# Optimization experiments

Measured on AMD Instinct MI355X. Metric: run time of the kernel, lower is better.

## Reference

```python
import jax, jax.numpy as jnp
import numpy as np

WAY = 5
SHOT = 5
SCALE = 10.0
EPS = 1e-8


def setup_inputs() -> dict:
    key = jax.random.key(0)
    k1, k2 = jax.random.split(key, 2)
    x = jax.random.normal(k1, (100, 512, 16, 16), dtype=jnp.float32)
    W = jax.random.normal(k2, (512, 512), dtype=jnp.float32) * 0.02  # 1x1 conv weight (outC, inC)
    b = jnp.zeros((512,), dtype=jnp.float32)
    return {"x": x, "W": W, "b": b}


def reference(x, W, b):
    B, C, H, Wd = x.shape
    # extract(): 1x1 conv -> softmax over flattened (C*H*W) per sample -> remask
    mask = jnp.einsum('bchw,oc->bohw', x, W) + b[None, :, None, None]
    mask = jax.nn.softmax(mask.reshape(B, -1), axis=1).reshape(B, C, H, Wd)
    x = x * mask
    # predict(): (way, shot+query, C, H, W)
    xv = x.reshape(WAY, -1, C, H, Wd)
    s = xv[:, :SHOT].mean(axis=(1, 3, 4))                    # (m=way, d=C) support prototypes
    q = xv[:, SHOT:].reshape(-1, C, H * Wd)                  # (n, d=C, f=H*W) queries
    # cosine_similarity over d, without materializing (n,m,d,f)
    qn = jnp.maximum(jnp.sqrt(jnp.sum(q * q, axis=1)), EPS)  # (n, f)
    sn = jnp.maximum(jnp.sqrt(jnp.sum(s * s, axis=1)), EPS)  # (m,)
    scores = jnp.einsum('ndf,md->nmf', q, s) / (qn[:, None, :] * sn[None, :, None])
    # softmax over classes (m), then mean over spatial positions f
    return jax.nn.softmax(SCALE * scores, axis=1).mean(axis=2)  # (n, way)
```

## Files before the change

### kernel.cpp

```cpp
#include <hip/hip_runtime.h>
#include <hip/hip_bf16.h>
#include <math.h>

typedef _Float16 half8 __attribute__((ext_vector_type(8)));
typedef float f32x4 __attribute__((ext_vector_type(4)));

#define BATCH 100
#define CH    512
#define HWP   256
#define SAMP  (CH * HWP)

__device__ __forceinline__ void async16(const void* g, void* l) {
  __builtin_amdgcn_global_load_lds(
      (const __attribute__((address_space(1))) unsigned int*)g,
      (__attribute__((address_space(3))) unsigned int*)l, 16, 0, 0);
}

__global__ __launch_bounds__(256) void k_txpose(const float* __restrict__ x,
                                               _Float16* __restrict__ xh) {
  __shared__ float tb[64][69];
  int bid  = blockIdx.x;
  int b    = bid >> 5;
  int tile = bid & 31;
  int c0 = (tile >> 2) << 6;
  int p0 = (tile & 3) << 6;
  int t = threadIdx.x;
  const float* xb = x + (size_t)b * SAMP;
#pragma unroll
  for (int it = 0; it < 4; it++) {
    int ch = it * 256 + t;
    int c  = ch >> 4;
    int pc = (ch & 15) << 2;
    float4 v = *(const float4*)(xb + (size_t)(c0 + c) * HWP + p0 + pc);
    tb[c][pc] = v.x; tb[c][pc + 1] = v.y; tb[c][pc + 2] = v.z; tb[c][pc + 3] = v.w;
  }
  __syncthreads();
  _Float16* xhb = xh + (size_t)b * SAMP;
#pragma unroll
  for (int it = 0; it < 2; it++) {
    int ch = it * 256 + t;
    int p  = ch >> 3;
    int ck = (ch & 7) << 3;
    half8 h;
#pragma unroll
    for (int j = 0; j < 8; j++) h[j] = (_Float16)tb[ck + j][p];
    *(half8*)(xhb + (size_t)(p0 + p) * CH + c0 + ck) = h;
  }
}

__global__ __launch_bounds__(256) void k_convw(const float* __restrict__ W,
                                              _Float16* __restrict__ Wh) {
  int base = blockIdx.x * 1024 + threadIdx.x;
#pragma unroll
  for (int j = 0; j < 4; j++) Wh[base + j * 256] = (_Float16)W[base + j * 256];
}

__global__ __launch_bounds__(256) void k_gemm(const _Float16* __restrict__ Wh,
                                             const _Float16* __restrict__ xh,
                                             const float* __restrict__ bias,
                                             float* __restrict__ eout,
                                             float* __restrict__ denom) {
  __shared__ __align__(16) _Float16 As[128 * 32];
  __shared__ __align__(16) _Float16 Bs[128 * 32];
  int bid   = blockIdx.x;
  int batch = bid >> 3;
  int sub   = bid & 7;
  int ot = sub & 3, pt = sub >> 2;
  int o0 = ot * 128, p0 = pt * 128;
  const _Float16* Bg = xh + (size_t)batch * SAMP;

  int t  = threadIdx.x;
  int wv = t >> 6, ln = t & 63;
  int qd = ln >> 4, r = ln & 15;
  int wm0 = (wv >> 1) * 64, wn0 = (wv & 1) * 64;

  f32x4 acc[4][4] = {};

  for (int kk = 0; kk < 512; kk += 32) {
#pragma unroll
    for (int it = 0; it < 2; it++) {
      int ch  = it * 256 + t;
      int row = ch >> 2;
      int qc  = ch & 3;
      char* la = (char*)As + (size_t)(it * 256 + wv * 64) * 16;
      char* lb = (char*)Bs + (size_t)(it * 256 + wv * 64) * 16;
      async16((const char*)(Wh + (size_t)(o0 + row) * 512 + kk + qc * 8), la);
      async16((const char*)(Bg + (size_t)(p0 + row) * 512 + kk + qc * 8), lb);
    }
    __syncthreads();
    half8 af[4], bf[4];
#pragma unroll
    for (int i = 0; i < 4; i++)
      af[i] = *(const half8*)(As + (wm0 + i * 16 + r) * 32 + qd * 8);
#pragma unroll
    for (int j = 0; j < 4; j++)
      bf[j] = *(const half8*)(Bs + (wn0 + j * 16 + r) * 32 + qd * 8);
#pragma unroll
    for (int i = 0; i < 4; i++)
#pragma unroll
      for (int j = 0; j < 4; j++)
        acc[i][j] = __builtin_amdgcn_mfma_f32_16x16x32_f16(af[i], bf[j], acc[i][j], 0, 0, 0);
    __syncthreads();
  }

  float* outb = eout + (size_t)batch * SAMP;
  float lsum = 0.f;
#pragma unroll
  for (int i = 0; i < 4; i++) {
#pragma unroll
    for (int rg = 0; rg < 4; rg++) {
      int o = o0 + wm0 + i * 16 + qd * 4 + rg;
      float bv = bias[o];
#pragma unroll
      for (int j = 0; j < 4; j++) {
        int p = p0 + wn0 + j * 16 + r;
        float e = __expf(acc[i][j][rg] + bv);
        outb[(size_t)o * HWP + p] = e;
        lsum += e;
      }
    }
  }
#pragma unroll
  for (int off = 32; off; off >>= 1) lsum += __shfl_down(lsum, off, 64);
  __shared__ float rs[4];
  if (ln == 0) rs[wv] = lsum;
  __syncthreads();
  if (t == 0) atomicAdd(&denom[batch], rs[0] + rs[1] + rs[2] + rs[3]);
}

__global__ __launch_bounds__(256) void k_proto(const float* __restrict__ x,
                                              const float* __restrict__ e,
                                              const float* __restrict__ denom,
                                              float* __restrict__ sproto) {
  int m = blockIdx.x / 512, c = blockIdx.x % 512;
  int t = threadIdx.x;
  float acc = 0.f;
  for (int j = 0; j < 5; j++) {
    int b = m * 20 + j;
    float invd = 1.0f / denom[b];
    size_t idx = (size_t)b * SAMP + (size_t)c * HWP + t;
    acc += x[idx] * e[idx] * invd;
  }
#pragma unroll
  for (int off = 32; off; off >>= 1) acc += __shfl_down(acc, off, 64);
  __shared__ float rs[4];
  if ((t & 63) == 0) rs[t >> 6] = acc;
  __syncthreads();
  if (t == 0) sproto[m * 512 + c] = (rs[0] + rs[1] + rs[2] + rs[3]) * (1.0f / 1280.0f);
}

__global__ __launch_bounds__(256) void k_sn(const float* __restrict__ sproto,
                                           float* __restrict__ pref) {
  int m = blockIdx.x, t = threadIdx.x;
  float v1 = sproto[m * 512 + t], v2 = sproto[m * 512 + 256 + t];
  float acc = v1 * v1 + v2 * v2;
#pragma unroll
  for (int off = 32; off; off >>= 1) acc += __shfl_down(acc, off, 64);
  __shared__ float rs[4];
  if ((t & 63) == 0) rs[t >> 6] = acc;
  __syncthreads();
  if (t == 0) {
    float sn = fmaxf(sqrtf(rs[0] + rs[1] + rs[2] + rs[3]), 1e-8f);
    pref[m] = 10.0f / sn;
  }
}

__global__ __launch_bounds__(256) void k_part(const float* __restrict__ x,
                                             const float* __restrict__ e,
                                             const float* __restrict__ sproto,
                                             float* __restrict__ part) {
  __shared__ float s_l[5 * 32];
  int n = blockIdx.x >> 4, gc = blockIdx.x & 15;
  int b = (n / 15) * 20 + 5 + (n % 15);
  int t = threadIdx.x;
  int c0 = gc * 32;
  if (t < 160) s_l[t] = sproto[(t / 32) * 512 + c0 + (t % 32)];
  __syncthreads();
  const float* xb = x + (size_t)b * SAMP + (size_t)c0 * HWP;
  const float* eb = e + (size_t)b * SAMP + (size_t)c0 * HWP;
  float dot[5] = {0, 0, 0, 0, 0}, qq = 0.f;
#pragma unroll 8
  for (int c = 0; c < 32; c++) {
    float u = xb[c * HWP + t] * eb[c * HWP + t];
    qq += u * u;
#pragma unroll
    for (int m = 0; m < 5; m++) dot[m] += u * s_l[m * 32 + c];
  }
  float* pp = part + (((size_t)n * 16 + gc) * 256 + t) * 6;
  pp[0] = dot[0]; pp[1] = dot[1]; pp[2] = dot[2];
  pp[3] = dot[3]; pp[4] = dot[4]; pp[5] = qq;
}

__global__ __launch_bounds__(256) void k_comb(const float* __restrict__ part,
                                             const float* __restrict__ pref,
                                             float* __restrict__ out) {
  int n = blockIdx.x, t = threadIdx.x;
  float dot[5] = {0, 0, 0, 0, 0}, qq = 0.f;
#pragma unroll
  for (int gc = 0; gc < 16; gc++) {
    const float* pp = part + (((size_t)n * 16 + gc) * 256 + t) * 6;
    dot[0] += pp[0]; dot[1] += pp[1]; dot[2] += pp[2];
    dot[3] += pp[3]; dot[4] += pp[4]; qq += pp[5];
  }
  float iqn = 1.0f / fmaxf(sqrtf(qq), 1e-20f);
  float sc[5], mx = -1e30f;
#pragma unroll
  for (int m = 0; m < 5; m++) { sc[m] = dot[m] * pref[m] * iqn; mx = fmaxf(mx, sc[m]); }
  float p[5], ssum = 0.f;
#pragma unroll
  for (int m = 0; m < 5; m++) { p[m] = __expf(sc[m] - mx); ssum += p[m]; }
  float rr = 1.0f / ssum;
#pragma unroll
  for (int m = 0; m < 5; m++) {
    float v = p[m] * rr;
#pragma unroll
    for (int off = 32; off; off >>= 1) v += __shfl_down(v, off, 64);
    p[m] = v;
  }
  __shared__ float rs[4][5];
  if ((t & 63) == 0) {
#pragma unroll
    for (int m = 0; m < 5; m++) rs[t >> 6][m] = p[m];
  }
  __syncthreads();
  if (t < 5) out[n * 5 + t] =
      (rs[0][t] + rs[1][t] + rs[2][t] + rs[3][t]) * (1.0f / 256.0f);
}

extern "C" void kernel_launch(void* const* d_in, const int* in_sizes, int n_in,
                              void* d_out, int out_size, void* d_ws, size_t ws_size,
                              hipStream_t stream) {
  const float* x    = (const float*)d_in[0];
  const float* W    = (const float*)d_in[1];
  const float* bias = (const float*)d_in[2];
  float* out = (float*)d_out;

  char* ws = (char*)d_ws;
  _Float16* xh     = (_Float16*)(ws + 0);
  float*    part   = (float*)   (ws + 0);
  _Float16* Wh     = (_Float16*)(ws + 26214400);
  float*    e      = (float*)   (ws + 26738688);
  float*    denom  = (float*)   (ws + 79167488);
  float*    sproto = (float*)   (ws + 79168000);
  float*    pref   = (float*)   (ws + 79178240);

  hipMemsetAsync(denom, 0, 512, stream);
  k_txpose <<<3200, 256, 0, stream>>>(x, xh);
  k_convw  <<<256,  256, 0, stream>>>(W, Wh);
  k_gemm   <<<800,  256, 0, stream>>>(Wh, xh, bias, e, denom);
  k_proto  <<<2560, 256, 0, stream>>>(x, e, denom, sproto);
  k_sn     <<<5,    256, 0, stream>>>(sproto, pref);
  k_part   <<<1200, 256, 0, stream>>>(x, e, sproto, part);
  k_comb   <<<75,   256, 0, stream>>>(part, pref, out);
}
```

Baseline: 152.8 us.

## Fuse x*exp(mask) into GEMM epilogue and store product as fp16

The GEMM epilogue now reloads the transposed fp16 x tile into an enlarged shared buffer and writes x times exp(logit) as fp16, instead of writing fp32 exp values. Downstream prototype and partial-dot kernels then read one fp16 tensor instead of two fp32 tensors. This cuts global traffic roughly fourfold for those stages. k_part is also regrouped to 64 channels per block with half as many blocks. It adds fp16 rounding of the unnormalized product, plus a larger shared-memory footprint in the GEMM that may lower occupancy.

```diff
diff --git a/kernel.cpp b/kernel.cpp
--- a/kernel.cpp
+++ b/kernel.cpp
@@ -58,10 +58,11 @@
 __global__ __launch_bounds__(256) void k_gemm(const _Float16* __restrict__ Wh,
                                              const _Float16* __restrict__ xh,
                                              const float* __restrict__ bias,
-                                             float* __restrict__ eout,
+                                             _Float16* __restrict__ u,
                                              float* __restrict__ denom) {
-  __shared__ __align__(16) _Float16 As[128 * 32];
-  __shared__ __align__(16) _Float16 Bs[128 * 32];
+  __shared__ __align__(16) _Float16 smem[128 * 136];
+  _Float16* As = smem;
+  _Float16* Bs = smem + 4096;
   int bid   = blockIdx.x;
   int batch = bid >> 3;
   int sub   = bid & 7;
@@ -103,20 +104,31 @@
     __syncthreads();
   }
 
-  float* outb = eout + (size_t)batch * SAMP;
+#pragma unroll
+  for (int it = 0; it < 8; it++) {
+    int ch = it * 256 + t;
+    int p  = ch >> 4;
+    int ck = ch & 15;
+    half8 v = *(const half8*)(Bg + (size_t)(p0 + p) * CH + o0 + ck * 8);
+    *(half8*)(smem + p * 136 + ck * 8) = v;
+  }
+  __syncthreads();
+
+  _Float16* outb = u + (size_t)batch * SAMP;
   float lsum = 0.f;
 #pragma unroll
   for (int i = 0; i < 4; i++) {
 #pragma unroll
     for (int rg = 0; rg < 4; rg++) {
-      int o = o0 + wm0 + i * 16 + qd * 4 + rg;
-      float bv = bias[o];
+      int ol = wm0 + i * 16 + qd * 4 + rg;
+      float bv = bias[o0 + ol];
 #pragma unroll
       for (int j = 0; j < 4; j++) {
-        int p = p0 + wn0 + j * 16 + r;
-        float e = __expf(acc[i][j][rg] + bv);
-        outb[(size_t)o * HWP + p] = e;
-        lsum += e;
+        int pl = wn0 + j * 16 + r;
+        float ev = __expf(acc[i][j][rg] + bv);
+        lsum += ev;
+        float xv = (float)smem[pl * 136 + ol];
+        outb[(size_t)(o0 + ol) * HWP + p0 + pl] = (_Float16)(xv * ev);
       }
     }
   }
@@ -128,8 +140,7 @@
   if (t == 0) atomicAdd(&denom[batch], rs[0] + rs[1] + rs[2] + rs[3]);
 }
 
-__global__ __launch_bounds__(256) void k_proto(const float* __restrict__ x,
-                                              const float* __restrict__ e,
+__global__ __launch_bounds__(256) void k_proto(const _Float16* __restrict__ u,
                                               const float* __restrict__ denom,
                                               float* __restrict__ sproto) {
   int m = blockIdx.x / 512, c = blockIdx.x % 512;
@@ -138,8 +149,7 @@
   for (int j = 0; j < 5; j++) {
     int b = m * 20 + j;
     float invd = 1.0f / denom[b];
-    size_t idx = (size_t)b * SAMP + (size_t)c * HWP + t;
-    acc += x[idx] * e[idx] * invd;
+    acc += (float)u[(size_t)b * SAMP + (size_t)c * HWP + t] * invd;
   }
 #pragma unroll
   for (int off = 32; off; off >>= 1) acc += __shfl_down(acc, off, 64);
@@ -165,28 +175,26 @@
   }
 }
 
-__global__ __launch_bounds__(256) void k_part(const float* __restrict__ x,
-                                             const float* __restrict__ e,
+__global__ __launch_bounds__(256) void k_part(const _Float16* __restrict__ u,
                                              const float* __restrict__ sproto,
                                              float* __restrict__ part) {
-  __shared__ float s_l[5 * 32];
-  int n = blockIdx.x >> 4, gc = blockIdx.x & 15;
+  __shared__ float s_l[5 * 64];
+  int n = blockIdx.x >> 3, gc = blockIdx.x & 7;
   int b = (n / 15) * 20 + 5 + (n % 15);
   int t = threadIdx.x;
-  int c0 = gc * 32;
-  if (t < 160) s_l[t] = sproto[(t / 32) * 512 + c0 + (t % 32)];
-  __syncthreads();
-  const float* xb = x + (size_t)b * SAMP + (size_t)c0 * HWP;
-  const float* eb = e + (size_t)b * SAMP + (size_t)c0 * HWP;
+  for (int i = t; i < 320; i += 256)
+    s_l[i] = sproto[(i >> 6) * 512 + gc * 64 + (i & 63)];
+  __syncthreads();
+  const _Float16* ub = u + (size_t)b * SAMP + (size_t)gc * 64 * HWP;
   float dot[5] = {0, 0, 0, 0, 0}, qq = 0.f;
 #pragma unroll 8
-  for (int c = 0; c < 32; c++) {
-    float u = xb[c * HWP + t] * eb[c * HWP + t];
-    qq += u * u;
-#pragma unroll
-    for (int m = 0; m < 5; m++) dot[m] += u * s_l[m * 32 + c];
-  }
-  float* pp = part + (((size_t)n * 16 + gc) * 256 + t) * 6;
+  for (int c = 0; c < 64; c++) {
+    float v = (float)ub[c * HWP + t];
+    qq += v * v;
+#pragma unroll
+    for (int m = 0; m < 5; m++) dot[m] += v * s_l[m * 64 + c];
+  }
+  float* pp = part + (((size_t)n * 8 + gc) * 256 + t) * 6;
   pp[0] = dot[0]; pp[1] = dot[1]; pp[2] = dot[2];
   pp[3] = dot[3]; pp[4] = dot[4]; pp[5] = qq;
 }
@@ -197,8 +205,8 @@
   int n = blockIdx.x, t = threadIdx.x;
   float dot[5] = {0, 0, 0, 0, 0}, qq = 0.f;
 #pragma unroll
-  for (int gc = 0; gc < 16; gc++) {
-    const float* pp = part + (((size_t)n * 16 + gc) * 256 + t) * 6;
+  for (int gc = 0; gc < 8; gc++) {
+    const float* pp = part + (((size_t)n * 8 + gc) * 256 + t) * 6;
     dot[0] += pp[0]; dot[1] += pp[1]; dot[2] += pp[2];
     dot[3] += pp[3]; dot[4] += pp[4]; qq += pp[5];
   }
@@ -239,17 +247,17 @@
   _Float16* xh     = (_Float16*)(ws + 0);
   float*    part   = (float*)   (ws + 0);
   _Float16* Wh     = (_Float16*)(ws + 26214400);
-  float*    e      = (float*)   (ws + 26738688);
-  float*    denom  = (float*)   (ws + 79167488);
-  float*    sproto = (float*)   (ws + 79168000);
-  float*    pref   = (float*)   (ws + 79178240);
+  _Float16* u      = (_Float16*)(ws + 26738688);
+  float*    denom  = (float*)   (ws + 52953088);
+  float*    sproto = (float*)   (ws + 52953600);
+  float*    pref   = (float*)   (ws + 52963840);
 
   hipMemsetAsync(denom, 0, 512, stream);
   k_txpose <<<3200, 256, 0, stream>>>(x, xh);
   k_convw  <<<256,  256, 0, stream>>>(W, Wh);
-  k_gemm   <<<800,  256, 0, stream>>>(Wh, xh, bias, e, denom);
-  k_proto  <<<2560, 256, 0, stream>>>(x, e, denom, sproto);
+  k_gemm   <<<800,  256, 0, stream>>>(Wh, xh, bias, u, denom);
+  k_proto  <<<2560, 256, 0, stream>>>(u, denom, sproto);
   k_sn     <<<5,    256, 0, stream>>>(sproto, pref);
-  k_part   <<<1200, 256, 0, stream>>>(x, e, sproto, part);
+  k_part   <<<600,  256, 0, stream>>>(u, sproto, part);
   k_comb   <<<75,   256, 0, stream>>>(part, pref, out);
 }
```

Result: faster. 142.1 us (-7.0%).
